# Kernel tuning notes

Hardware: AMD Instinct MI355X
Metric: run time of the kernel (lower is better)

Reference implementation:

```python
import jax, jax.numpy as jnp
import numpy as np

C = 32          # middle_channels
N_DOWN = 13     # layers 2..14, stride 2
DENSITY = 0.01  # nnz fraction of the 2048x2048 sparse matrix


def _conv(x, w):
    # centered SAME conv; inactive sites hold zeros so they contribute nothing,
    # matching MinkowskiConvolution's sum over existing neighbor coordinates.
    return jax.lax.conv_general_dilated(
        x, w, window_strides=(1, 1), padding='SAME',
        dimension_numbers=('NHWC', 'HWIO', 'NHWC'))


def _downsample_mask(mask):
    # ME stride-2 output coords = stride-quantized input coords -> OR over 2x2 block
    return jax.lax.reduce_window(mask, 0.0, jax.lax.max, (1, 2, 2), (1, 2, 2), 'SAME')


def _layer(x, mask, w, stride):
    y = _conv(x, w)
    if stride > 1:
        y = y[:, ::stride, ::stride, :]   # value at quantized coordinate u
        mask = _downsample_mask(mask)
    y = jax.nn.relu(y) * mask[..., None]  # ReLU on active sites, keep inactive = 0
    return y, mask


def _global_avg_pool(x, mask):
    cnt = jnp.maximum(jnp.sum(mask, axis=(1, 2)), 1.0)  # number of active coords
    return jnp.sum(x, axis=(1, 2)) / cnt[:, None]       # [B, C]


def setup_inputs() -> dict:
    key = jax.random.key(0)
    ks = jax.random.split(key, 8)
    H = W = 2048
    mask = (jax.random.uniform(ks[0], (1, H, W)) < DENSITY).astype(jnp.float32)
    x = jax.random.normal(ks[1], (1, H, W, 1), dtype=jnp.float32) * mask[..., None]
    # kaiming_normal fan_out (nonlinearity='relu') for conv kernels, bias=False in ME
    w1 = jax.random.normal(ks[2], (5, 5, 1, C), dtype=jnp.float32) * np.float32((2.0 / (5 * 5 * C)) ** 0.5)
    ws = jax.random.normal(ks[3], (N_DOWN, 3, 3, C, C), dtype=jnp.float32) * np.float32((2.0 / (3 * 3 * C)) ** 0.5)
    wm1 = jax.random.normal(ks[4], (C * 14, 256), dtype=jnp.float32) * np.float32((1.0 / (C * 14)) ** 0.5)
    bm1 = jnp.zeros((256,), jnp.float32)
    wm2 = jax.random.normal(ks[5], (256, 128), dtype=jnp.float32) * np.float32((1.0 / 256) ** 0.5)
    bm2 = jnp.zeros((128,), jnp.float32)
    return {'x': x, 'mask': mask, 'w1': w1, 'ws': ws,
            'wm1': wm1, 'bm1': bm1, 'wm2': wm2, 'bm2': bm2}


def reference(x, mask, w1, ws, wm1, bm1, wm2, bm2):
    y, m = _layer(x, mask, w1, stride=1)          # layer1: k=5, s=1
    pools = [_global_avg_pool(y, m)]
    for i in range(N_DOWN):                       # layers 2..14: k=3, s=2
        y, m = _layer(y, m, ws[i], stride=2)
        pools.append(_global_avg_pool(y, m))
    feat = jnp.concatenate(pools, axis=-1)        # [B, 32*14]
    h = jax.nn.relu(feat @ wm1 + bm1)
    return h @ wm2 + bm2                          # [B, 128]
```

## Files before the change

### kernel.cpp

```cpp
#include <hip/hip_runtime.h>

#define NLVL 14
#define NSHARD 16

struct ZeroArgs { unsigned long long zoff[13]; };

__device__ __forceinline__ float fma4(float4 v, float4 w, float acc) {
    acc = fmaf(v.x, w.x, acc);
    acc = fmaf(v.y, w.y, acc);
    acc = fmaf(v.z, w.z, acc);
    return fmaf(v.w, w.w, acc);
}

__device__ __forceinline__ int block_scan_base(int mycnt, int* gcnt, int& myoff) {
    __shared__ int wsum[4];
    __shared__ int base;
    int lane = threadIdx.x & 63, wid = threadIdx.x >> 6;
    int scan = mycnt;
    #pragma unroll
    for (int d = 1; d < 64; d <<= 1) {
        int tv = __shfl_up(scan, d, 64);
        if (lane >= d) scan += tv;
    }
    if (lane == 63) wsum[wid] = scan;
    __syncthreads();
    if (threadIdx.x == 0) {
        int tot = 0;
        #pragma unroll
        for (int i = 0; i < 4; i++) { int tv = wsum[i]; wsum[i] = tot; tot += tv; }
        base = tot ? atomicAdd(gcnt, tot) : 0;
    }
    __syncthreads();
    myoff = wsum[wid] + scan - mycnt;
    return base;
}

__device__ void compact0_tile(const float4* __restrict__ mask4, int* __restrict__ idxmap,
                              int* __restrict__ coords, int* __restrict__ cnt, int cap, int tile) {
    int t = threadIdx.x;
    int g0 = tile * 1024 + t;
    float4 m[4];
    #pragma unroll
    for (int j = 0; j < 4; j++) m[j] = mask4[g0 + j * 256];
    int pr[16];
    int mycnt = 0;
    #pragma unroll
    for (int j = 0; j < 4; j++) {
        pr[4 * j + 0] = m[j].x > 0.5f;
        pr[4 * j + 1] = m[j].y > 0.5f;
        pr[4 * j + 2] = m[j].z > 0.5f;
        pr[4 * j + 3] = m[j].w > 0.5f;
        mycnt += pr[4 * j] + pr[4 * j + 1] + pr[4 * j + 2] + pr[4 * j + 3];
    }
    int myoff;
    int base = block_scan_base(mycnt, cnt, myoff);
    int slot = base + myoff;
    #pragma unroll
    for (int j = 0; j < 4; j++) {
        int e0 = (g0 + j * 256) << 2;
        int wv[4];
        #pragma unroll
        for (int k = 0; k < 4; k++) {
            wv[k] = -1;
            if (pr[4 * j + k]) {
                int sl = slot++;
                if (sl < cap) { wv[k] = sl; coords[sl] = e0 + k; }
            }
        }
        *(int4*)(idxmap + e0) = make_int4(wv[0], wv[1], wv[2], wv[3]);
    }
}

__device__ void down_nbr(const int* __restrict__ idx_in, int HinB,
                         int* __restrict__ idx_out, int* __restrict__ nbr_out,
                         int* __restrict__ cnt_out, int HoutB, int cap_out,
                         int zofs, int bb) {
    int Hout = 1 << HoutB, Hin = 1 << HinB;
    int S = Hout * Hout;
    int S4 = (S + 3) >> 2;
    int o4 = bb * 256 + threadIdx.x;
    int e0 = o4 << 2;
    int jv[4][9];
    int pr[4] = {0, 0, 0, 0};
    #pragma unroll
    for (int k = 0; k < 4; k++)
        #pragma unroll
        for (int tap = 0; tap < 9; tap++) jv[k][tap] = -1;
    if (o4 < S4) {
        if (HoutB >= 2) {
            int r = e0 >> HoutB, c0 = e0 & (Hout - 1);
            int w[3][12];
            #pragma unroll
            for (int a = 0; a < 3; a++) {
                int rr = 2 * r + a - 1;
                bool rok = (unsigned)rr < (unsigned)Hin;
                const int* rowp = idx_in + ((size_t)(rok ? rr : 0) << HinB) + 2 * c0;
                int4 L = (rok && c0 > 0) ? *(const int4*)(rowp - 4) : make_int4(-1, -1, -1, -1);
                int4 M = rok ? *(const int4*)rowp : make_int4(-1, -1, -1, -1);
                int4 R = rok ? *(const int4*)(rowp + 4) : make_int4(-1, -1, -1, -1);
                w[a][0] = L.x; w[a][1] = L.y; w[a][2]  = L.z; w[a][3]  = L.w;
                w[a][4] = M.x; w[a][5] = M.y; w[a][6]  = M.z; w[a][7]  = M.w;
                w[a][8] = R.x; w[a][9] = R.y; w[a][10] = R.z; w[a][11] = R.w;
            }
            #pragma unroll
            for (int k = 0; k < 4; k++) {
                #pragma unroll
                for (int a = 0; a < 3; a++)
                    #pragma unroll
                    for (int b = 0; b < 3; b++)
                        jv[k][a * 3 + b] = w[a][2 * k + b + 3];
                pr[k] = ((jv[k][4] & jv[k][5] & jv[k][7] & jv[k][8]) >= 0);
            }
        } else {
            #pragma unroll
            for (int k = 0; k < 4; k++) {
                int p = e0 + k;
                if (p < S) {
                    int r = p >> HoutB, c = p & (Hout - 1);
                    #pragma unroll
                    for (int a = 0; a < 3; a++)
                        #pragma unroll
                        for (int b = 0; b < 3; b++) {
                            int rr = 2 * r + a - 1, cc = 2 * c + b - 1;
                            if ((unsigned)rr < (unsigned)Hin && (unsigned)cc < (unsigned)Hin)
                                jv[k][a * 3 + b] = idx_in[((size_t)rr << HinB) + cc];
                        }
                    pr[k] = ((jv[k][4] & jv[k][5] & jv[k][7] & jv[k][8]) >= 0);
                }
            }
        }
    }
    int mycnt = pr[0] + pr[1] + pr[2] + pr[3];
    int myoff;
    int base = block_scan_base(mycnt, cnt_out, myoff);
    int slot = base + myoff;
    int wv[4] = {-1, -1, -1, -1};
    #pragma unroll
    for (int k = 0; k < 4; k++) {
        if (pr[k]) {
            int sl = slot++;
            if (sl < cap_out) {
                wv[k] = sl;
                #pragma unroll
                for (int tap = 0; tap < 9; tap++) {
                    int j = jv[k][tap];
                    nbr_out[sl * 9 + tap] = (j < 0) ? zofs : (j << 7);
                }
            }
        }
    }
    if (o4 < S4) {
        if (S >= 4) *(int4*)(idx_out + e0) = make_int4(wv[0], wv[1], wv[2], wv[3]);
        else {
            #pragma unroll
            for (int k = 0; k < 4; k++) if (e0 + k < S) idx_out[e0 + k] = wv[k];
        }
    }
}

__device__ void conv_bs(const char* __restrict__ vprevb, const float* __restrict__ wlvl,
                        const int* __restrict__ nbr, int n,
                        float* __restrict__ vals, float* __restrict__ poolp,
                        int b0, int nbk, int shard) {
    __shared__ int s_j[144];
    __shared__ __align__(16) float s_in[144 * 32];
    int t = threadIdx.x;
    int ciq = t & 7, coh = (t >> 3) & 15, sp = t >> 7;
    float4 wreg[9][2];
    #pragma unroll
    for (int tap = 0; tap < 9; tap++) {
        wreg[tap][0] = *(const float4*)(wlvl + ((tap * 32 + coh) << 5) + (ciq << 2));
        wreg[tap][1] = *(const float4*)(wlvl + ((tap * 32 + coh + 16) << 5) + (ciq << 2));
    }
    float ps0 = 0.f, ps1 = 0.f;
    int ngr = (n + 15) >> 4;
    for (int grp = b0; grp < ngr; grp += nbk) {
        __syncthreads();
        if (t < 144) {
            int gi = grp * 144 + t;
            s_j[t] = (gi < n * 9) ? nbr[gi] : 0;
        }
        __syncthreads();
        #pragma unroll
        for (int i = t; i < 1152; i += 256) {
            int row = i >> 3, q = i & 7;
            *(float4*)&s_in[(row << 5) + (q << 2)] =
                *(const float4*)(vprevb + s_j[row] + (q << 4));
        }
        __syncthreads();
        #pragma unroll
        for (int gp = 0; gp < 8; gp++) {
            int g = gp * 2 + sp;
            int s = (grp << 4) + g;
            float4 v[9];
            #pragma unroll
            for (int tap = 0; tap < 9; tap++)
                v[tap] = *(const float4*)&s_in[((g * 9 + tap) << 5) + (ciq << 2)];
            float a0 = 0.f, a1 = 0.f;
            #pragma unroll
            for (int tap = 0; tap < 9; tap++) {
                a0 = fma4(v[tap], wreg[tap][0], a0);
                a1 = fma4(v[tap], wreg[tap][1], a1);
            }
            a0 += __shfl_xor(a0, 1); a0 += __shfl_xor(a0, 2); a0 += __shfl_xor(a0, 4);
            a1 += __shfl_xor(a1, 1); a1 += __shfl_xor(a1, 2); a1 += __shfl_xor(a1, 4);
            if (ciq == 0 && s < n) {
                float r0 = fmaxf(a0, 0.f), r1 = fmaxf(a1, 0.f);
                vals[((size_t)s << 5) + coh] = r0;
                vals[((size_t)s << 5) + coh + 16] = r1;
                ps0 += r0; ps1 += r1;
            }
        }
    }
    if (ciq == 0 && (ps0 != 0.f || ps1 != 0.f)) {
        atomicAdd(&poolp[shard * 448 + coh], ps0);
        atomicAdd(&poolp[shard * 448 + coh + 16], ps1);
    }
}

__device__ void conv0_bs(const float* __restrict__ x, const float* __restrict__ w1,
                         const int* __restrict__ coords0, int n,
                         float* __restrict__ vals0, float* __restrict__ poolp,
                         int b0, int nbk, int shard) {
    __shared__ float lw[800];
    __shared__ float lx[8][28];
    __shared__ float red[256];
    int t = threadIdx.x;
    for (int i = t; i < 800; i += 256) lw[i] = w1[i];
    int sl = t >> 5, ch = t & 31;
    float psum = 0.f;
    int ngr = (n + 7) >> 3;
    for (int grp = b0; grp < ngr; grp += nbk) {
        __syncthreads();
        if (t < 200) {
            int slot = t / 25, tap = t - slot * 25;
            int s = (grp << 3) + slot;
            float v = 0.f;
            if (s < n) {
                int p = coords0[s];
                int r = p >> 11, c = p & 2047;
                int a = tap / 5, b = tap - a * 5;
                int rr = r + a - 2, cc = c + b - 2;
                if ((unsigned)rr < 2048u && (unsigned)cc < 2048u)
                    v = x[(rr << 11) + cc];
            }
            lx[slot][tap] = v;
        }
        __syncthreads();
        int s = (grp << 3) + sl;
        float acc = 0.f;
        #pragma unroll
        for (int tap = 0; tap < 25; tap++)
            acc = fmaf(lx[sl][tap], lw[tap * 32 + ch], acc);
        if (s < n) {
            float r0 = fmaxf(acc, 0.f);
            vals0[((size_t)s << 5) + ch] = r0;
            psum += r0;
        }
    }
    __syncthreads();
    red[t] = psum;
    __syncthreads();
    if (t < 32) {
        float tot = 0.f;
        #pragma unroll
        for (int q = 0; q < 8; q++) tot += red[t + 32 * q];
        if (tot != 0.f) atomicAdd(&poolp[shard * 448 + t], tot);
    }
}

__global__ __launch_bounds__(256) void k_f0(
    const float4* __restrict__ mask4, int* __restrict__ idxmap,
    int* __restrict__ coords, int* __restrict__ cnt, int cap,
    const float* __restrict__ w, float* __restrict__ wt,
    char* __restrict__ wsbase, ZeroArgs za) {
    if (blockIdx.x == 1492) {
        for (int i = threadIdx.x; i < 13 * 32; i += 256)
            *(float*)(wsbase + za.zoff[i >> 5] + ((i & 31) << 2)) = 0.f;
        return;
    }
    if (blockIdx.x >= 1024) {
        int t = (int)(blockIdx.x - 1024) * 256 + threadIdx.x;
        if (t < 13 * 9 * 32 * 32) {
            int ci = t & 31, co = (t >> 5) & 31, tp = t >> 10;
            wt[(tp << 10) + (co << 5) + ci] = w[(tp << 10) + (ci << 5) + co];
        }
        return;
    }
    compact0_tile(mask4, idxmap, coords, cnt, cap, blockIdx.x);
}

__global__ __launch_bounds__(256) void k_f1(
    const int* __restrict__ idx0, int* __restrict__ idx1, int* __restrict__ nbr1,
    int* __restrict__ cnt1, int cap1, int zofs1,
    const float* __restrict__ x, const float* __restrict__ w1,
    const int* __restrict__ coords0, const int* __restrict__ cnt0, int cap0,
    float* __restrict__ vals0, float* __restrict__ poolp,
    const float* __restrict__ wm1, const float* __restrict__ wm2, float* __restrict__ dummy) {
    if (blockIdx.x < 1024) {
        down_nbr(idx0, 11, idx1, nbr1, cnt1, 10, cap1, zofs1, blockIdx.x);
        return;
    }
    if (blockIdx.x >= 5120) {
        int t = (int)(blockIdx.x - 5120) * 256 + threadIdx.x;
        const float4* a = (const float4*)wm1;
        const float4* b = (const float4*)wm2;
        float acc = 0.f;
        for (int i = t; i < 28672; i += 6144) { float4 v = a[i]; acc += v.x + v.y + v.z + v.w; }
        for (int i = t; i < 8192; i += 6144)  { float4 v = b[i]; acc += v.x + v.y + v.z + v.w; }
        if (acc == 1234.56789f) dummy[0] = acc;
        return;
    }
    int n = *cnt0; if (n > cap0) n = cap0;
    conv0_bs(x, w1, coords0, n, vals0, poolp, blockIdx.x - 1024, 4096, blockIdx.x & (NSHARD - 1));
}

__global__ __launch_bounds__(256) void k_flevel(
    int downB,
    const int* __restrict__ idx_in, int HinB,
    int* __restrict__ idx_out, int* __restrict__ nbr_out, int* __restrict__ cnt_out,
    int HoutB, int cap_out, int zofs,
    const char* __restrict__ vprevb, const float* __restrict__ wlvl,
    const int* __restrict__ nbr_c, const int* __restrict__ cnt_c, int cap_c,
    float* __restrict__ vals_c, float* __restrict__ poolp) {
    if ((int)blockIdx.x < downB) {
        down_nbr(idx_in, HinB, idx_out, nbr_out, cnt_out, HoutB, cap_out, zofs, blockIdx.x);
        return;
    }
    int n = *cnt_c; if (n > cap_c) n = cap_c;
    conv_bs(vprevb, wlvl, nbr_c, n, vals_c, poolp,
            blockIdx.x - downB, gridDim.x - downB, blockIdx.x & (NSHARD - 1));
}

__global__ __launch_bounds__(1024) void k_tail(
    const int* __restrict__ cnt, const float* __restrict__ poolsh,
    const char* __restrict__ vals9b, const int* __restrict__ nbr10,
    const int* __restrict__ idx10, const float* __restrict__ wt,
    const float* __restrict__ wm1, const float* __restrict__ bm1,
    const float* __restrict__ wm2, const float* __restrict__ bm2,
    float* __restrict__ out) {
    __shared__ __align__(16) float v10[128];
    __shared__ float v11[32], v12[32], v13[32];
    __shared__ float feat[448], h[256], part[1024];
    __shared__ int s_i10[4], s_n10;
    int t = threadIdx.x;
    int ciq = t & 7, co = (t >> 3) & 31, s = t >> 8;
    int ciq16 = ciq << 4;
    if (t == 0) s_n10 = cnt[10];
    if (t < 4) s_i10[t] = idx10[t];
    __syncthreads();
    int n10 = s_n10; if (n10 > 4) n10 = 4;
    {
        const float* wl = wt + (size_t)9 * 9216;
        float4 wreg[9];
        #pragma unroll
        for (int tap = 0; tap < 9; tap++)
            wreg[tap] = *(const float4*)(wl + ((tap * 32 + co) << 5) + (ciq << 2));
        bool live = s < n10;
        int sb = live ? s : 0;
        float a0 = 0.f;
        #pragma unroll
        for (int tap = 0; tap < 9; tap++)
            a0 = fma4(*(const float4*)(vals9b + nbr10[sb * 9 + tap] + ciq16), wreg[tap], a0);
        a0 += __shfl_xor(a0, 1); a0 += __shfl_xor(a0, 2); a0 += __shfl_xor(a0, 4);
        if (ciq == 0 && live) v10[s * 32 + co] = fmaxf(a0, 0.f);
    }
    __syncthreads();
    int i10[4] = {s_i10[0], s_i10[1], s_i10[2], s_i10[3]};
    int nbr11[9];
    #pragma unroll
    for (int tap = 0; tap < 9; tap++) {
        int a = tap / 3, b = tap - a * 3;
        int rr = a - 1, cc = b - 1;
        nbr11[tap] = ((unsigned)rr < 2u && (unsigned)cc < 2u) ? i10[rr * 2 + cc] : -1;
    }
    int n11 = ((nbr11[4] & nbr11[5] & nbr11[7] & nbr11[8]) >= 0) ? 1 : 0;
    if (s == 0) {
        const float* wl = wt + (size_t)10 * 9216;
        float a0 = 0.f;
        #pragma unroll
        for (int tap = 0; tap < 9; tap++) {
            int j = nbr11[tap];
            if (j >= 0) {
                float4 wv = *(const float4*)(wl + ((tap * 32 + co) << 5) + (ciq << 2));
                a0 = fma4(*(const float4*)(&v10[(j << 5) + (ciq << 2)]), wv, a0);
            }
        }
        a0 += __shfl_xor(a0, 1); a0 += __shfl_xor(a0, 2); a0 += __shfl_xor(a0, 4);
        if (ciq == 0) v11[co] = n11 ? fmaxf(a0, 0.f) : 0.f;
    }
    __syncthreads();
    if (s == 0) {
        const float* wl = wt + (size_t)11 * 9216;
        float4 wv = *(const float4*)(wl + ((4 * 32 + co) << 5) + (ciq << 2));
        float a0 = n11 ? fma4(*(const float4*)(&v11[ciq << 2]), wv, 0.f) : 0.f;
        a0 += __shfl_xor(a0, 1); a0 += __shfl_xor(a0, 2); a0 += __shfl_xor(a0, 4);
        if (ciq == 0) v12[co] = n11 ? fmaxf(a0, 0.f) : 0.f;
    }
    __syncthreads();
    if (s == 0) {
        const float* wl = wt + (size_t)12 * 9216;
        float4 wv = *(const float4*)(wl + ((4 * 32 + co) << 5) + (ciq << 2));
        float a0 = n11 ? fma4(*(const float4*)(&v12[ciq << 2]), wv, 0.f) : 0.f;
        a0 += __shfl_xor(a0, 1); a0 += __shfl_xor(a0, 2); a0 += __shfl_xor(a0, 4);
        if (ciq == 0) v13[co] = n11 ? fmaxf(a0, 0.f) : 0.f;
    }
    __syncthreads();
    if (t < 320) {
        float sum = 0.f;
        #pragma unroll
        for (int sh = 0; sh < NSHARD; sh++) sum += poolsh[sh * 448 + t];
        float c = (float)cnt[t >> 5]; if (c < 1.f) c = 1.f;
        feat[t] = sum / c;
    }
    if (t < 32) {
        float s10 = 0.f;
        for (int q = 0; q < n10; q++) s10 += v10[q * 32 + t];
        float c10 = (float)n10; if (c10 < 1.f) c10 = 1.f;
        feat[320 + t] = s10 / c10;
        feat[352 + t] = n11 ? v11[t] : 0.f;
        feat[384 + t] = n11 ? v12[t] : 0.f;
        feat[416 + t] = n11 ? v13[t] : 0.f;
    }
    __syncthreads();
    {
        int j = t & 255, chunk = t >> 8;
        float acc = (chunk == 0) ? bm1[j] : 0.f;
        int k0 = chunk * 112;
        #pragma unroll 8
        for (int k = k0; k < k0 + 112; k++) acc = fmaf(feat[k], wm1[k * 256 + j], acc);
        part[t] = acc;
    }
    __syncthreads();
    if (t < 256)
        h[t] = fmaxf(part[t] + part[t + 256] + part[t + 512] + part[t + 768], 0.f);
    __syncthreads();
    {
        int j2 = t & 127, c2 = t >> 7;
        float a2 = (c2 == 0) ? bm2[j2] : 0.f;
        int kk0 = c2 * 32;
        #pragma unroll 8
        for (int k = kk0; k < kk0 + 32; k++) a2 = fmaf(h[k], wm2[k * 128 + j2], a2);
        part[t] = a2;
    }
    __syncthreads();
    if (t < 128) {
        float sum = 0.f;
        #pragma unroll
        for (int c = 0; c < 8; c++) sum += part[t + 128 * c];
        out[t] = sum;
    }
}

extern "C" void kernel_launch(void* const* d_in, const int* in_sizes, int n_in,
                              void* d_out, int out_size, void* d_ws, size_t ws_size,
                              hipStream_t stream) {
    const float* x    = (const float*)d_in[0];
    const float* mask = (const float*)d_in[1];
    const float* w1   = (const float*)d_in[2];
    const float* wsrc = (const float*)d_in[3];
    const float* wm1  = (const float*)d_in[4];
    const float* bm1  = (const float*)d_in[5];
    const float* wm2  = (const float*)d_in[6];
    const float* bm2  = (const float*)d_in[7];
    float* out = (float*)d_out;
    char* ws = (char*)d_ws;

    static const int Hb[NLVL]   = {11, 10, 9, 8, 7, 6, 5, 4, 3, 2, 1, 0, 0, 0};
    static const int caps[NLVL] = {45056, 43008, 43008, 34816, 16384, 4096,
                                   1024, 256, 64, 16, 4, 1, 1, 1};

    size_t pool_off = 256;
    size_t wt_off = 32768;
    size_t off = wt_off + (size_t)13 * 9 * 1024 * 4;
    off = (off + 255) & ~(size_t)255;
    size_t coord0_off = off; off += (size_t)caps[0] * 4; off = (off + 255) & ~(size_t)255;
    size_t idx_off[NLVL], nbr_off[NLVL], val_off[NLVL];
    for (int l = 0; l < NLVL; l++) {
        size_t S = (size_t)(1 << Hb[l]) * (1 << Hb[l]);
        size_t sb = S * 4; if (sb < 16) sb = 16;
        idx_off[l] = off; off += sb; off = (off + 255) & ~(size_t)255;
        if (l >= 1) { nbr_off[l] = off; off += (size_t)caps[l] * 36; off = (off + 255) & ~(size_t)255; }
        else nbr_off[l] = 0;
        val_off[l] = off; off += (size_t)(caps[l] + 1) * 128; off = (off + 255) & ~(size_t)255;
    }

    int* cnt = (int*)ws;
    float* poolsh = (float*)(ws + pool_off);
    float* dummy = (float*)(ws + 128);
    float* wt = (float*)(ws + wt_off);

    ZeroArgs za;
    for (int l = 0; l < 13; l++) za.zoff[l] = val_off[l] + (size_t)caps[l] * 128;

    hipMemsetAsync(ws, 0, 32768, stream);

    k_f0<<<1493, 256, 0, stream>>>(
        (const float4*)mask, (int*)(ws + idx_off[0]), (int*)(ws + coord0_off),
        cnt, caps[0], wsrc, wt, ws, za);

    k_f1<<<5144, 256, 0, stream>>>(
        (const int*)(ws + idx_off[0]), (int*)(ws + idx_off[1]), (int*)(ws + nbr_off[1]),
        cnt + 1, caps[1], caps[0] * 128,
        x, w1, (const int*)(ws + coord0_off), cnt, caps[0],
        (float*)(ws + val_off[0]), poolsh, wm1, wm2, dummy);

    for (int i = 2; i <= 10; i++) {
        int lc = i - 1;
        int Hout = 1 << Hb[i];
        int S4 = (Hout * Hout + 3) >> 2;
        int downB = (S4 + 255) >> 8; if (downB < 1) downB = 1;
        int convB = (caps[lc] + 15) >> 4;
        k_flevel<<<downB + convB, 256, 0, stream>>>(
            downB,
            (const int*)(ws + idx_off[i - 1]), Hb[i - 1],
            (int*)(ws + idx_off[i]), (int*)(ws + nbr_off[i]), cnt + i, Hb[i], caps[i],
            caps[i - 1] * 128,
            (const char*)(ws + val_off[lc - 1]), wt + (size_t)(lc - 1) * 9216,
            (const int*)(ws + nbr_off[lc]), cnt + lc, caps[lc],
            (float*)(ws + val_off[lc]), poolsh + lc * 32);
    }

    k_tail<<<1, 1024, 0, stream>>>(
        cnt, poolsh,
        (const char*)(ws + val_off[9]), (const int*)(ws + nbr_off[10]),
        (const int*)(ws + idx_off[10]), wt,
        wm1, bm1, wm2, bm2, out);
}
```

Before: 267.1 us.

## Fuse multi-kernel pipeline into one cooperative persistent kernel with grid syncs

Replaces the sequence of per-level kernel launches (f0, f1, nine level kernels, tail) with a single cooperative kernel of 256 blocks that loops over levels, separated by grid-wide syncs. The aim is to remove launch gaps and the kernel-boundary cost between the many small late levels. In exchange, the early large levels now run on a fixed 256-block grid with strided tile loops rather than thousands of blocks, so they may lose parallelism. Each grid sync also has a cost. The original launch path is kept as a fallback, and the tail is reworked to use 256 threads.

```diff
diff --git a/kernel.cpp b/kernel.cpp
--- a/kernel.cpp
+++ b/kernel.cpp
@@ -1,9 +1,22 @@
 #include <hip/hip_runtime.h>
+#include <hip/hip_cooperative_groups.h>
+
+namespace cg = cooperative_groups;
 
 #define NLVL 14
 #define NSHARD 16
 
 struct ZeroArgs { unsigned long long zoff[13]; };
+
+struct AllArgs {
+    const float4* mask4;
+    const float* x; const float* w1; const float* wsrc;
+    const float* wm1; const float* bm1; const float* wm2; const float* bm2;
+    float* out; char* ws;
+    unsigned long long idx_off[NLVL], nbr_off[NLVL], val_off[NLVL];
+    unsigned long long coord0_off, wt_off;
+    int caps[NLVL];
+};
 
 __device__ __forceinline__ float fma4(float4 v, float4 w, float acc) {
     acc = fmaf(v.x, w.x, acc);
@@ -269,6 +282,186 @@
     }
 }
 
+__device__ void tail_256(const int* __restrict__ cnt, const float* __restrict__ poolsh,
+                         const char* __restrict__ vals9b, const int* __restrict__ nbr10,
+                         const int* __restrict__ idx10, const float* __restrict__ wt,
+                         const float* __restrict__ wm1, const float* __restrict__ bm1,
+                         const float* __restrict__ wm2, const float* __restrict__ bm2,
+                         float* __restrict__ out) {
+    __shared__ __align__(16) float v10[128];
+    __shared__ float v11[32], v12[32], v13[32];
+    __shared__ float feat[448], h[256];
+    __shared__ int s_i10[4], s_n10;
+    int t = threadIdx.x;
+    int ciq = t & 7, co = (t >> 3) & 31;
+    int ciq16 = ciq << 4;
+    if (t == 0) s_n10 = cnt[10];
+    if (t < 4) s_i10[t] = idx10[t];
+    __syncthreads();
+    int n10 = s_n10; if (n10 > 4) n10 = 4;
+    {
+        const float* wl = wt + (size_t)9 * 9216;
+        float4 wreg[9];
+        #pragma unroll
+        for (int tap = 0; tap < 9; tap++)
+            wreg[tap] = *(const float4*)(wl + ((tap * 32 + co) << 5) + (ciq << 2));
+        for (int s = 0; s < n10; s++) {
+            float a0 = 0.f;
+            #pragma unroll
+            for (int tap = 0; tap < 9; tap++)
+                a0 = fma4(*(const float4*)(vals9b + nbr10[s * 9 + tap] + ciq16), wreg[tap], a0);
+            a0 += __shfl_xor(a0, 1); a0 += __shfl_xor(a0, 2); a0 += __shfl_xor(a0, 4);
+            if (ciq == 0) v10[s * 32 + co] = fmaxf(a0, 0.f);
+        }
+    }
+    __syncthreads();
+    int i10[4] = {s_i10[0], s_i10[1], s_i10[2], s_i10[3]};
+    int nbr11[9];
+    #pragma unroll
+    for (int tap = 0; tap < 9; tap++) {
+        int a = tap / 3, b = tap - a * 3;
+        int rr = a - 1, cc = b - 1;
+        nbr11[tap] = ((unsigned)rr < 2u && (unsigned)cc < 2u) ? i10[rr * 2 + cc] : -1;
+    }
+    int n11 = ((nbr11[4] & nbr11[5] & nbr11[7] & nbr11[8]) >= 0) ? 1 : 0;
+    {
+        const float* wl = wt + (size_t)10 * 9216;
+        float a0 = 0.f;
+        #pragma unroll
+        for (int tap = 0; tap < 9; tap++) {
+            int j = nbr11[tap];
+            if (j >= 0) {
+                float4 wv = *(const float4*)(wl + ((tap * 32 + co) << 5) + (ciq << 2));
+                a0 = fma4(*(const float4*)(&v10[(j << 5) + (ciq << 2)]), wv, a0);
+            }
+        }
+        a0 += __shfl_xor(a0, 1); a0 += __shfl_xor(a0, 2); a0 += __shfl_xor(a0, 4);
+        if (ciq == 0) v11[co] = n11 ? fmaxf(a0, 0.f) : 0.f;
+    }
+    __syncthreads();
+    {
+        const float* wl = wt + (size_t)11 * 9216;
+        float4 wv = *(const float4*)(wl + ((4 * 32 + co) << 5) + (ciq << 2));
+        float a0 = n11 ? fma4(*(const float4*)(&v11[ciq << 2]), wv, 0.f) : 0.f;
+        a0 += __shfl_xor(a0, 1); a0 += __shfl_xor(a0, 2); a0 += __shfl_xor(a0, 4);
+        if (ciq == 0) v12[co] = n11 ? fmaxf(a0, 0.f) : 0.f;
+    }
+    __syncthreads();
+    {
+        const float* wl = wt + (size_t)12 * 9216;
+        float4 wv = *(const float4*)(wl + ((4 * 32 + co) << 5) + (ciq << 2));
+        float a0 = n11 ? fma4(*(const float4*)(&v12[ciq << 2]), wv, 0.f) : 0.f;
+        a0 += __shfl_xor(a0, 1); a0 += __shfl_xor(a0, 2); a0 += __shfl_xor(a0, 4);
+        if (ciq == 0) v13[co] = n11 ? fmaxf(a0, 0.f) : 0.f;
+    }
+    __syncthreads();
+    for (int k = t; k < 320; k += 256) {
+        float sum = 0.f;
+        #pragma unroll
+        for (int sh = 0; sh < NSHARD; sh++) sum += poolsh[sh * 448 + k];
+        float c = (float)cnt[k >> 5]; if (c < 1.f) c = 1.f;
+        feat[k] = sum / c;
+    }
+    if (t < 32) {
+        float s10 = 0.f;
+        for (int q = 0; q < n10; q++) s10 += v10[q * 32 + t];
+        float c10 = (float)n10; if (c10 < 1.f) c10 = 1.f;
+        feat[320 + t] = s10 / c10;
+        feat[352 + t] = n11 ? v11[t] : 0.f;
+        feat[384 + t] = n11 ? v12[t] : 0.f;
+        feat[416 + t] = n11 ? v13[t] : 0.f;
+    }
+    __syncthreads();
+    {
+        float acc = bm1[t];
+        #pragma unroll 8
+        for (int k = 0; k < 448; k++) acc = fmaf(feat[k], wm1[k * 256 + t], acc);
+        h[t] = fmaxf(acc, 0.f);
+    }
+    __syncthreads();
+    if (t < 128) {
+        float o = bm2[t];
+        #pragma unroll 8
+        for (int k = 0; k < 256; k++) o = fmaf(h[k], wm2[k * 128 + t], o);
+        out[t] = o;
+    }
+}
+
+__global__ __launch_bounds__(256) void k_all(AllArgs A) {
+    cg::grid_group gg = cg::this_grid();
+    const int bid = blockIdx.x;
+    const int t = threadIdx.x;
+    char* ws = A.ws;
+    int* cnt = (int*)ws;
+    float* poolsh = (float*)(ws + 256);
+    float* wt = (float*)(ws + A.wt_off);
+    int* coords0 = (int*)(ws + A.coord0_off);
+    constexpr int Hb[NLVL] = {11, 10, 9, 8, 7, 6, 5, 4, 3, 2, 1, 0, 0, 0};
+
+    for (int tile = bid; tile < 1024; tile += 256)
+        compact0_tile(A.mask4, (int*)(ws + A.idx_off[0]), coords0, cnt, A.caps[0], tile);
+    for (int i = bid * 256 + t; i < 13 * 9 * 32 * 32; i += 256 * 256) {
+        int ci = i & 31, co = (i >> 5) & 31, tp = i >> 10;
+        wt[(tp << 10) + (co << 5) + ci] = A.wsrc[(tp << 10) + (ci << 5) + co];
+    }
+    if (bid == 0) {
+        for (int i = t; i < 13 * 32; i += 256) {
+            int l = i >> 5;
+            *(float*)(ws + A.val_off[l] + (size_t)A.caps[l] * 128 + ((i & 31) << 2)) = 0.f;
+        }
+    }
+    {
+        float acc = 0.f;
+        const float4* a = (const float4*)A.wm1;
+        const float4* b = (const float4*)A.wm2;
+        for (int i = bid * 256 + t; i < 28672; i += 65536) { float4 v = a[i]; acc += v.x + v.y + v.z + v.w; }
+        for (int i = bid * 256 + t; i < 8192; i += 65536)  { float4 v = b[i]; acc += v.x + v.y + v.z + v.w; }
+        if (acc == 1234.56789f) *(float*)(ws + 128) = acc;
+    }
+    gg.sync();
+
+    {
+        int n0 = cnt[0]; if (n0 > A.caps[0]) n0 = A.caps[0];
+        if (bid < 64) {
+            for (int tile = bid; tile < 1024; tile += 64)
+                down_nbr((const int*)(ws + A.idx_off[0]), 11,
+                         (int*)(ws + A.idx_off[1]), (int*)(ws + A.nbr_off[1]),
+                         cnt + 1, 10, A.caps[1], A.caps[0] * 128, tile);
+        } else {
+            conv0_bs(A.x, A.w1, coords0, n0,
+                     (float*)(ws + A.val_off[0]), poolsh, bid - 64, 192, bid & (NSHARD - 1));
+        }
+    }
+    gg.sync();
+
+    for (int l = 2; l <= 10; l++) {
+        int S = 1 << (2 * Hb[l]);
+        int S4 = (S + 3) >> 2;
+        int tiles = (S4 + 255) >> 8; if (tiles < 1) tiles = 1;
+        int downB = tiles < 128 ? tiles : 128;
+        int lc = l - 1;
+        int n = cnt[lc]; if (n > A.caps[lc]) n = A.caps[lc];
+        if (bid < downB) {
+            for (int tile = bid; tile < tiles; tile += downB)
+                down_nbr((const int*)(ws + A.idx_off[l - 1]), Hb[l - 1],
+                         (int*)(ws + A.idx_off[l]), (int*)(ws + A.nbr_off[l]),
+                         cnt + l, Hb[l], A.caps[l], A.caps[l - 1] * 128, tile);
+        } else {
+            conv_bs((const char*)(ws + A.val_off[lc - 1]), wt + (size_t)(lc - 1) * 9216,
+                    (const int*)(ws + A.nbr_off[lc]), n,
+                    (float*)(ws + A.val_off[lc]), poolsh + lc * 32,
+                    bid - downB, 256 - downB, bid & (NSHARD - 1));
+        }
+        gg.sync();
+    }
+
+    if (bid == 0)
+        tail_256(cnt, poolsh,
+                 (const char*)(ws + A.val_off[9]), (const int*)(ws + A.nbr_off[10]),
+                 (const int*)(ws + A.idx_off[10]), wt,
+                 A.wm1, A.bm1, A.wm2, A.bm2, A.out);
+}
+
 __global__ __launch_bounds__(256) void k_f0(
     const float4* __restrict__ mask4, int* __restrict__ idxmap,
     int* __restrict__ coords, int* __restrict__ cnt, int cap,
@@ -332,124 +525,14 @@
             blockIdx.x - downB, gridDim.x - downB, blockIdx.x & (NSHARD - 1));
 }
 
-__global__ __launch_bounds__(1024) void k_tail(
+__global__ __launch_bounds__(256) void k_tailk(
     const int* __restrict__ cnt, const float* __restrict__ poolsh,
     const char* __restrict__ vals9b, const int* __restrict__ nbr10,
     const int* __restrict__ idx10, const float* __restrict__ wt,
     const float* __restrict__ wm1, const float* __restrict__ bm1,
     const float* __restrict__ wm2, const float* __restrict__ bm2,
     float* __restrict__ out) {
-    __shared__ __align__(16) float v10[128];
-    __shared__ float v11[32], v12[32], v13[32];
-    __shared__ float feat[448], h[256], part[1024];
-    __shared__ int s_i10[4], s_n10;
-    int t = threadIdx.x;
-    int ciq = t & 7, co = (t >> 3) & 31, s = t >> 8;
-    int ciq16 = ciq << 4;
-    if (t == 0) s_n10 = cnt[10];
-    if (t < 4) s_i10[t] = idx10[t];
-    __syncthreads();
-    int n10 = s_n10; if (n10 > 4) n10 = 4;
-    {
-        const float* wl = wt + (size_t)9 * 9216;
-        float4 wreg[9];
-        #pragma unroll
-        for (int tap = 0; tap < 9; tap++)
-            wreg[tap] = *(const float4*)(wl + ((tap * 32 + co) << 5) + (ciq << 2));
-        bool live = s < n10;
-        int sb = live ? s : 0;
-        float a0 = 0.f;
-        #pragma unroll
-        for (int tap = 0; tap < 9; tap++)
-            a0 = fma4(*(const float4*)(vals9b + nbr10[sb * 9 + tap] + ciq16), wreg[tap], a0);
-        a0 += __shfl_xor(a0, 1); a0 += __shfl_xor(a0, 2); a0 += __shfl_xor(a0, 4);
-        if (ciq == 0 && live) v10[s * 32 + co] = fmaxf(a0, 0.f);
-    }
-    __syncthreads();
-    int i10[4] = {s_i10[0], s_i10[1], s_i10[2], s_i10[3]};
-    int nbr11[9];
-    #pragma unroll
-    for (int tap = 0; tap < 9; tap++) {
-        int a = tap / 3, b = tap - a * 3;
-        int rr = a - 1, cc = b - 1;
-        nbr11[tap] = ((unsigned)rr < 2u && (unsigned)cc < 2u) ? i10[rr * 2 + cc] : -1;
-    }
-    int n11 = ((nbr11[4] & nbr11[5] & nbr11[7] & nbr11[8]) >= 0) ? 1 : 0;
-    if (s == 0) {
-        const float* wl = wt + (size_t)10 * 9216;
-        float a0 = 0.f;
-        #pragma unroll
-        for (int tap = 0; tap < 9; tap++) {
-            int j = nbr11[tap];
-            if (j >= 0) {
-                float4 wv = *(const float4*)(wl + ((tap * 32 + co) << 5) + (ciq << 2));
-                a0 = fma4(*(const float4*)(&v10[(j << 5) + (ciq << 2)]), wv, a0);
-            }
-        }
-        a0 += __shfl_xor(a0, 1); a0 += __shfl_xor(a0, 2); a0 += __shfl_xor(a0, 4);
-        if (ciq == 0) v11[co] = n11 ? fmaxf(a0, 0.f) : 0.f;
-    }
-    __syncthreads();
-    if (s == 0) {
-        const float* wl = wt + (size_t)11 * 9216;
-        float4 wv = *(const float4*)(wl + ((4 * 32 + co) << 5) + (ciq << 2));
-        float a0 = n11 ? fma4(*(const float4*)(&v11[ciq << 2]), wv, 0.f) : 0.f;
-        a0 += __shfl_xor(a0, 1); a0 += __shfl_xor(a0, 2); a0 += __shfl_xor(a0, 4);
-        if (ciq == 0) v12[co] = n11 ? fmaxf(a0, 0.f) : 0.f;
-    }
-    __syncthreads();
-    if (s == 0) {
-        const float* wl = wt + (size_t)12 * 9216;
-        float4 wv = *(const float4*)(wl + ((4 * 32 + co) << 5) + (ciq << 2));
-        float a0 = n11 ? fma4(*(const float4*)(&v12[ciq << 2]), wv, 0.f) : 0.f;
-        a0 += __shfl_xor(a0, 1); a0 += __shfl_xor(a0, 2); a0 += __shfl_xor(a0, 4);
-        if (ciq == 0) v13[co] = n11 ? fmaxf(a0, 0.f) : 0.f;
-    }
-    __syncthreads();
-    if (t < 320) {
-        float sum = 0.f;
-        #pragma unroll
-        for (int sh = 0; sh < NSHARD; sh++) sum += poolsh[sh * 448 + t];
-        float c = (float)cnt[t >> 5]; if (c < 1.f) c = 1.f;
-        feat[t] = sum / c;
-    }
-    if (t < 32) {
-        float s10 = 0.f;
-        for (int q = 0; q < n10; q++) s10 += v10[q * 32 + t];
-        float c10 = (float)n10; if (c10 < 1.f) c10 = 1.f;
-        feat[320 + t] = s10 / c10;
-        feat[352 + t] = n11 ? v11[t] : 0.f;
-        feat[384 + t] = n11 ? v12[t] : 0.f;
-        feat[416 + t] = n11 ? v13[t] : 0.f;
-    }
-    __syncthreads();
-    {
-        int j = t & 255, chunk = t >> 8;
-        float acc = (chunk == 0) ? bm1[j] : 0.f;
-        int k0 = chunk * 112;
-        #pragma unroll 8
-        for (int k = k0; k < k0 + 112; k++) acc = fmaf(feat[k], wm1[k * 256 + j], acc);
-        part[t] = acc;
-    }
-    __syncthreads();
-    if (t < 256)
-        h[t] = fmaxf(part[t] + part[t + 256] + part[t + 512] + part[t + 768], 0.f);
-    __syncthreads();
-    {
-        int j2 = t & 127, c2 = t >> 7;
-        float a2 = (c2 == 0) ? bm2[j2] : 0.f;
-        int kk0 = c2 * 32;
-        #pragma unroll 8
-        for (int k = kk0; k < kk0 + 32; k++) a2 = fmaf(h[k], wm2[k * 128 + j2], a2);
-        part[t] = a2;
-    }
-    __syncthreads();
-    if (t < 128) {
-        float sum = 0.f;
-        #pragma unroll
-        for (int c = 0; c < 8; c++) sum += part[t + 128 * c];
-        out[t] = sum;
-    }
+    tail_256(cnt, poolsh, vals9b, nbr10, idx10, wt, wm1, bm1, wm2, bm2, out);
 }
 
 extern "C" void kernel_launch(void* const* d_in, const int* in_sizes, int n_in,
@@ -470,7 +553,6 @@
     static const int caps[NLVL] = {45056, 43008, 43008, 34816, 16384, 4096,
                                    1024, 256, 64, 16, 4, 1, 1, 1};
 
-    size_t pool_off = 256;
     size_t wt_off = 32768;
     size_t off = wt_off + (size_t)13 * 9 * 1024 * 4;
     off = (off + 255) & ~(size_t)255;
@@ -486,14 +568,36 @@
     }
 
     int* cnt = (int*)ws;
-    float* poolsh = (float*)(ws + pool_off);
+    float* poolsh = (float*)(ws + 256);
     float* dummy = (float*)(ws + 128);
     float* wt = (float*)(ws + wt_off);
 
+    hipMemsetAsync(ws, 0, 32768, stream);
+
+    AllArgs A;
+    A.mask4 = (const float4*)mask;
+    A.x = x; A.w1 = w1; A.wsrc = wsrc;
+    A.wm1 = wm1; A.bm1 = bm1; A.wm2 = wm2; A.bm2 = bm2;
+    A.out = out; A.ws = ws;
+    for (int l = 0; l < NLVL; l++) {
+        A.idx_off[l] = idx_off[l]; A.nbr_off[l] = nbr_off[l]; A.val_off[l] = val_off[l];
+        A.caps[l] = caps[l];
+    }
+    A.coord0_off = coord0_off; A.wt_off = wt_off;
+
+    bool coop_done = false;
+    int nbPerCU = 0;
+    hipError_t qe = hipOccupancyMaxActiveBlocksPerMultiprocessor(&nbPerCU, k_all, 256, 0);
+    if (qe == hipSuccess && nbPerCU >= 1) {
+        void* kargs[] = { &A };
+        hipError_t le = hipLaunchCooperativeKernel((const void*)k_all, dim3(256), dim3(256),
+                                                   kargs, 0, stream);
+        if (le == hipSuccess) coop_done = true;
+    }
+    if (coop_done) return;
+
     ZeroArgs za;
     for (int l = 0; l < 13; l++) za.zoff[l] = val_off[l] + (size_t)caps[l] * 128;
-
-    hipMemsetAsync(ws, 0, 32768, stream);
 
     k_f0<<<1493, 256, 0, stream>>>(
         (const float4*)mask, (int*)(ws + idx_off[0]), (int*)(ws + coord0_off),
@@ -521,7 +625,7 @@
             (float*)(ws + val_off[lc]), poolsh + lc * 32);
     }
 
-    k_tail<<<1, 1024, 0, stream>>>(
+    k_tailk<<<1, 256, 0, stream>>>(
         cnt, poolsh,
         (const char*)(ws + val_off[9]), (const int*)(ws + nbr_off[10]),
         (const int*)(ws + idx_off[10]), wt,
```

After: 399.2 us. 1.49x slower.

## Fold the last two level launches into the single-block tail kernel

Applied to the files above, without the earlier changes.

The level loop now stops at 8, so levels 8 through 10 (convs, neighbor building via ballot compaction, and pooling) run inside the one-block tail kernel using shared memory instead of two more grid launches. This is meant to remove the launch and inter-kernel sync cost of small late levels that do little work. In exchange, one 1024-thread block does up to 64 sites of conv serially and needs much more shared memory, which limits parallelism on that stage.

```diff
diff --git a/kernel.cpp b/kernel.cpp
--- a/kernel.cpp
+++ b/kernel.cpp
@@ -334,39 +334,143 @@
 
 __global__ __launch_bounds__(1024) void k_tail(
     const int* __restrict__ cnt, const float* __restrict__ poolsh,
-    const char* __restrict__ vals9b, const int* __restrict__ nbr10,
-    const int* __restrict__ idx10, const float* __restrict__ wt,
+    const char* __restrict__ vals7b, const int* __restrict__ nbr8,
+    const int* __restrict__ idx8, const float* __restrict__ wt,
     const float* __restrict__ wm1, const float* __restrict__ bm1,
     const float* __restrict__ wm2, const float* __restrict__ bm2,
     float* __restrict__ out) {
+    __shared__ __align__(16) float sv7[8224];
+    __shared__ __align__(16) float v8[2048];
+    __shared__ __align__(16) float v9[512];
     __shared__ __align__(16) float v10[128];
     __shared__ float v11[32], v12[32], v13[32];
-    __shared__ float feat[448], h[256], part[1024];
-    __shared__ int s_i10[4], s_n10;
+    __shared__ float pol8[32], pol9[32];
+    __shared__ int snbr8[576];
+    __shared__ int idx9s[16], nbr9s[144];
+    __shared__ int idx10s[4], nbr10s[36];
+    __shared__ float feat[448], h[256], part[1024], red[256];
+    __shared__ int s_n[4];
     int t = threadIdx.x;
-    int ciq = t & 7, co = (t >> 3) & 31, s = t >> 8;
-    int ciq16 = ciq << 4;
-    if (t == 0) s_n10 = cnt[10];
-    if (t < 4) s_i10[t] = idx10[t];
-    __syncthreads();
-    int n10 = s_n10; if (n10 > 4) n10 = 4;
+    int ciq = t & 7, co = (t >> 3) & 31, sp = t >> 8;
+
+    {
+        const float4* g = (const float4*)vals7b;
+        float4* l = (float4*)sv7;
+        for (int i = t; i < 2048; i += 1024) l[i] = g[i];
+        if (t < 32) sv7[8192 + t] = 0.f;
+    }
+    if (t == 0) { int n = cnt[8]; s_n[0] = (n > 64) ? 64 : n; }
+    if (t >= 64 && t < 640) snbr8[t - 64] = nbr8[t - 64];
+    __syncthreads();
+    int n8 = s_n[0];
+    {
+        const float* wl = wt + (size_t)7 * 9216;
+        float4 wreg[9];
+        #pragma unroll
+        for (int tap = 0; tap < 9; tap++)
+            wreg[tap] = *(const float4*)(wl + ((tap * 32 + co) << 5) + (ciq << 2));
+        for (int s = sp; s < n8; s += 4) {
+            float a0 = 0.f;
+            #pragma unroll
+            for (int tap = 0; tap < 9; tap++) {
+                int off = snbr8[s * 9 + tap];
+                a0 = fma4(*(const float4*)&sv7[(off >> 2) + (ciq << 2)], wreg[tap], a0);
+            }
+            a0 += __shfl_xor(a0, 1); a0 += __shfl_xor(a0, 2); a0 += __shfl_xor(a0, 4);
+            if (ciq == 0) v8[s * 32 + co] = fmaxf(a0, 0.f);
+        }
+    }
+    __syncthreads();
+    if (t < 256) {
+        int g = t >> 5, ch = t & 31;
+        float s = 0.f;
+        for (int q = g; q < n8; q += 8) s += v8[q * 32 + ch];
+        red[t] = s;
+    }
+    __syncthreads();
+    if (t < 32) { float tot = 0.f; for (int g = 0; g < 8; g++) tot += red[t + 32 * g]; pol8[t] = tot; }
+    if (t >= 960 && t < 976) {
+        int q = t - 960;
+        int r = q >> 2, c = q & 3;
+        int jv[9];
+        #pragma unroll
+        for (int tap = 0; tap < 9; tap++) {
+            int a = tap / 3, b = tap - a * 3;
+            int rr = 2 * r + a - 1, cc = 2 * c + b - 1;
+            jv[tap] = ((unsigned)rr < 8u && (unsigned)cc < 8u) ? idx8[rr * 8 + cc] : -1;
+        }
+        int pred = ((jv[4] & jv[5] & jv[7] & jv[8]) >= 0);
+        unsigned long long b = __ballot(pred);
+        int lane = t & 63;
+        int slot = (int)__popcll(b & ((1ull << lane) - 1ull));
+        idx9s[q] = pred ? slot : -1;
+        if (pred)
+            #pragma unroll
+            for (int tap = 0; tap < 9; tap++) nbr9s[slot * 9 + tap] = jv[tap];
+        if (q == 0) s_n[1] = (int)__popcll(b);
+    }
+    __syncthreads();
+    int n9 = s_n[1];
+    {
+        const float* wl = wt + (size_t)8 * 9216;
+        float4 wreg[9];
+        #pragma unroll
+        for (int tap = 0; tap < 9; tap++)
+            wreg[tap] = *(const float4*)(wl + ((tap * 32 + co) << 5) + (ciq << 2));
+        for (int s = sp; s < n9; s += 4) {
+            float a0 = 0.f;
+            #pragma unroll
+            for (int tap = 0; tap < 9; tap++) {
+                int j = nbr9s[s * 9 + tap];
+                if (j >= 0) a0 = fma4(*(const float4*)&v8[(j << 5) + (ciq << 2)], wreg[tap], a0);
+            }
+            a0 += __shfl_xor(a0, 1); a0 += __shfl_xor(a0, 2); a0 += __shfl_xor(a0, 4);
+            if (ciq == 0) v9[s * 32 + co] = fmaxf(a0, 0.f);
+        }
+    }
+    __syncthreads();
+    if (t < 32) { float s = 0.f; for (int q = 0; q < n9; q++) s += v9[q * 32 + t]; pol9[t] = s; }
+    if (t >= 960 && t < 964) {
+        int q = t - 960;
+        int r = q >> 1, c = q & 1;
+        int jv[9];
+        #pragma unroll
+        for (int tap = 0; tap < 9; tap++) {
+            int a = tap / 3, b = tap - a * 3;
+            int rr = 2 * r + a - 1, cc = 2 * c + b - 1;
+            jv[tap] = ((unsigned)rr < 4u && (unsigned)cc < 4u) ? idx9s[rr * 4 + cc] : -1;
+        }
+        int pred = ((jv[4] & jv[5] & jv[7] & jv[8]) >= 0);
+        unsigned long long b = __ballot(pred);
+        int lane = t & 63;
+        int slot = (int)__popcll(b & ((1ull << lane) - 1ull));
+        idx10s[q] = pred ? slot : -1;
+        if (pred)
+            #pragma unroll
+            for (int tap = 0; tap < 9; tap++) nbr10s[slot * 9 + tap] = jv[tap];
+        if (q == 0) s_n[2] = (int)__popcll(b);
+    }
+    __syncthreads();
+    int n10 = s_n[2];
     {
         const float* wl = wt + (size_t)9 * 9216;
         float4 wreg[9];
         #pragma unroll
         for (int tap = 0; tap < 9; tap++)
             wreg[tap] = *(const float4*)(wl + ((tap * 32 + co) << 5) + (ciq << 2));
-        bool live = s < n10;
-        int sb = live ? s : 0;
-        float a0 = 0.f;
-        #pragma unroll
-        for (int tap = 0; tap < 9; tap++)
-            a0 = fma4(*(const float4*)(vals9b + nbr10[sb * 9 + tap] + ciq16), wreg[tap], a0);
-        a0 += __shfl_xor(a0, 1); a0 += __shfl_xor(a0, 2); a0 += __shfl_xor(a0, 4);
-        if (ciq == 0 && live) v10[s * 32 + co] = fmaxf(a0, 0.f);
-    }
-    __syncthreads();
-    int i10[4] = {s_i10[0], s_i10[1], s_i10[2], s_i10[3]};
+        for (int s = sp; s < n10; s += 4) {
+            float a0 = 0.f;
+            #pragma unroll
+            for (int tap = 0; tap < 9; tap++) {
+                int j = nbr10s[s * 9 + tap];
+                if (j >= 0) a0 = fma4(*(const float4*)&v9[(j << 5) + (ciq << 2)], wreg[tap], a0);
+            }
+            a0 += __shfl_xor(a0, 1); a0 += __shfl_xor(a0, 2); a0 += __shfl_xor(a0, 4);
+            if (ciq == 0) v10[s * 32 + co] = fmaxf(a0, 0.f);
+        }
+    }
+    __syncthreads();
+    int i10[4] = {idx10s[0], idx10s[1], idx10s[2], idx10s[3]};
     int nbr11[9];
     #pragma unroll
     for (int tap = 0; tap < 9; tap++) {
@@ -375,7 +479,7 @@
         nbr11[tap] = ((unsigned)rr < 2u && (unsigned)cc < 2u) ? i10[rr * 2 + cc] : -1;
     }
     int n11 = ((nbr11[4] & nbr11[5] & nbr11[7] & nbr11[8]) >= 0) ? 1 : 0;
-    if (s == 0) {
+    if (sp == 0) {
         const float* wl = wt + (size_t)10 * 9216;
         float a0 = 0.f;
         #pragma unroll
@@ -390,7 +494,7 @@
         if (ciq == 0) v11[co] = n11 ? fmaxf(a0, 0.f) : 0.f;
     }
     __syncthreads();
-    if (s == 0) {
+    if (sp == 0) {
         const float* wl = wt + (size_t)11 * 9216;
         float4 wv = *(const float4*)(wl + ((4 * 32 + co) << 5) + (ciq << 2));
         float a0 = n11 ? fma4(*(const float4*)(&v11[ciq << 2]), wv, 0.f) : 0.f;
@@ -398,7 +502,7 @@
         if (ciq == 0) v12[co] = n11 ? fmaxf(a0, 0.f) : 0.f;
     }
     __syncthreads();
-    if (s == 0) {
+    if (sp == 0) {
         const float* wl = wt + (size_t)12 * 9216;
         float4 wv = *(const float4*)(wl + ((4 * 32 + co) << 5) + (ciq << 2));
         float a0 = n11 ? fma4(*(const float4*)(&v12[ciq << 2]), wv, 0.f) : 0.f;
@@ -406,12 +510,20 @@
         if (ciq == 0) v13[co] = n11 ? fmaxf(a0, 0.f) : 0.f;
     }
     __syncthreads();
-    if (t < 320) {
+    if (t < 256) {
         float sum = 0.f;
         #pragma unroll
         for (int sh = 0; sh < NSHARD; sh++) sum += poolsh[sh * 448 + t];
         float c = (float)cnt[t >> 5]; if (c < 1.f) c = 1.f;
         feat[t] = sum / c;
+    } else if (t < 288) {
+        int ch = t - 256;
+        float c = (float)(n8 > 0 ? n8 : 1);
+        feat[t] = pol8[ch] / c;
+    } else if (t < 320) {
+        int ch = t - 288;
+        float c = (float)(n9 > 0 ? n9 : 1);
+        feat[t] = pol9[ch] / c;
     }
     if (t < 32) {
         float s10 = 0.f;
@@ -470,7 +582,6 @@
     static const int caps[NLVL] = {45056, 43008, 43008, 34816, 16384, 4096,
                                    1024, 256, 64, 16, 4, 1, 1, 1};
 
-    size_t pool_off = 256;
     size_t wt_off = 32768;
     size_t off = wt_off + (size_t)13 * 9 * 1024 * 4;
     off = (off + 255) & ~(size_t)255;
@@ -486,14 +597,14 @@
     }
 
     int* cnt = (int*)ws;
-    float* poolsh = (float*)(ws + pool_off);
+    float* poolsh = (float*)(ws + 256);
     float* dummy = (float*)(ws + 128);
     float* wt = (float*)(ws + wt_off);
 
+    hipMemsetAsync(ws, 0, 32768, stream);
+
     ZeroArgs za;
     for (int l = 0; l < 13; l++) za.zoff[l] = val_off[l] + (size_t)caps[l] * 128;
-
-    hipMemsetAsync(ws, 0, 32768, stream);
 
     k_f0<<<1493, 256, 0, stream>>>(
         (const float4*)mask, (int*)(ws + idx_off[0]), (int*)(ws + coord0_off),
@@ -505,7 +616,7 @@
         x, w1, (const int*)(ws + coord0_off), cnt, caps[0],
         (float*)(ws + val_off[0]), poolsh, wm1, wm2, dummy);
 
-    for (int i = 2; i <= 10; i++) {
+    for (int i = 2; i <= 8; i++) {
         int lc = i - 1;
         int Hout = 1 << Hb[i];
         int S4 = (Hout * Hout + 3) >> 2;
@@ -523,7 +634,7 @@
 
     k_tail<<<1, 1024, 0, stream>>>(
         cnt, poolsh,
-        (const char*)(ws + val_off[9]), (const int*)(ws + nbr_off[10]),
-        (const int*)(ws + idx_off[10]), wt,
+        (const char*)(ws + val_off[7]), (const int*)(ws + nbr_off[8]),
+        (const int*)(ws + idx_off[8]), wt,
         wm1, bm1, wm2, bm2, out);
 }
```

Result: slower. 273.3 us (+2.3%).
